# Kernel optimization log

Hardware: AMD Instinct MI355X
Metric: run time of the kernel (lower is better)

The kernel has to match this reference:

```python
import jax, jax.numpy as jnp
import numpy as np

B, T, D = 4096, 200, 64
NEG_INF = -(2.0 ** 32) + 1.0  # matches tf paddings constant


def setup_inputs() -> dict:
    key = jax.random.key(0)
    ks = jax.random.split(key, 12)
    queries = jax.random.normal(ks[0], (B, D), dtype=jnp.float32)
    keys = jax.random.normal(ks[1], (B, T, D), dtype=jnp.float32)
    keys_length = jax.random.randint(ks[2], (B,), 0, 200, dtype=jnp.int32)
    # attention MLP params (glorot-ish scale)
    W1 = jax.random.normal(ks[3], (4 * D, 16), dtype=jnp.float32) * (1.0 / np.sqrt(4 * D))
    b1 = jnp.zeros((16,), dtype=jnp.float32)
    W2 = jax.random.normal(ks[4], (16, 8), dtype=jnp.float32) * (1.0 / np.sqrt(16))
    b2 = jnp.zeros((8,), dtype=jnp.float32)
    W3 = jax.random.normal(ks[5], (8, 1), dtype=jnp.float32) * (1.0 / np.sqrt(8))
    b3 = jnp.zeros((1,), dtype=jnp.float32)
    W4 = jax.random.normal(ks[6], (D, D), dtype=jnp.float32) * (1.0 / np.sqrt(D))
    b4 = jnp.zeros((D,), dtype=jnp.float32)
    return {"queries": queries, "keys": keys, "keys_length": keys_length,
            "W1": W1, "b1": b1, "W2": W2, "b2": b2, "W3": W3, "b3": b3,
            "W4": W4, "b4": b4}


def reference(queries, keys, keys_length, W1, b1, W2, b2, W3, b3, W4, b4):
    Bq, Tq, Dq = keys.shape
    # tile queries across time: [B, T, D]
    q = jnp.broadcast_to(queries[:, None, :], (Bq, Tq, Dq))
    # DIN feature construction: [B, T, 4D]
    din_all = jnp.concatenate([q, keys, q - keys, q * keys], axis=-1)
    # tiny MLP scorer
    x = jax.nn.sigmoid(jnp.einsum('btf,fh->bth', din_all, W1) + b1)
    x = jax.nn.sigmoid(jnp.einsum('bth,hk->btk', x, W2) + b2)
    scores = (jnp.einsum('btk,ko->bto', x, W3) + b3)[..., 0]  # [B, T]
    # mask invalid history positions
    mask = jnp.arange(Tq, dtype=keys_length.dtype)[None, :] < keys_length[:, None]
    scores = jnp.where(mask, scores, NEG_INF)
    scores = scores / (Dq ** 0.5)  # scaling applied after masking, as in tf code
    attn = jax.nn.softmax(scores, axis=-1)  # [B, T]
    out = jnp.einsum('bt,btd->bd', attn, keys)  # weighted sum of keys
    out = out @ W4 + b4  # [B, D]
    return out
```

## Files before the change

kernel.cpp:

```cpp
#include <hip/hip_runtime.h>
#include <math.h>

#define TT 200
#define MTS 72

typedef __attribute__((ext_vector_type(8))) short bf16x8;
typedef __attribute__((ext_vector_type(4))) float f32x4;

__device__ __forceinline__ float sigmoidf_(float x) {
    return 1.0f / (1.0f + __expf(-x));
}
__device__ __forceinline__ short f2bf(float x) {
    unsigned u = __float_as_uint(x);
    u += 0x7fff + ((u >> 16) & 1);
    return (short)(u >> 16);
}
__device__ __forceinline__ float bf2f(short s) {
    return __uint_as_float(((unsigned)(unsigned short)s) << 16);
}
__device__ __forceinline__ void build_hi(float4 v0, float4 v1, bf16x8& hi) {
    float xs[8] = {v0.x, v0.y, v0.z, v0.w, v1.x, v1.y, v1.z, v1.w};
    #pragma unroll
    for (int j = 0; j < 8; j++) hi[j] = f2bf(xs[j]);
}

__global__ __launch_bounds__(256) void din_attn_flash(
    const float* __restrict__ queries,
    const float* __restrict__ keys,
    const int*   __restrict__ keys_length,
    const float* __restrict__ W1,
    const float* __restrict__ b1,
    const float* __restrict__ W2,
    const float* __restrict__ b2,
    const float* __restrict__ W3,
    const float* __restrict__ b3,
    const float* __restrict__ W4,
    const float* __restrict__ b4,
    float* __restrict__ out,
    int Bn)
{
    __shared__ __align__(16) short MtHi[4][16 * MTS];
    __shared__ __align__(16) short MtLo[4][16 * MTS];
    __shared__ __align__(16) float w2s[16 * 8];
    __shared__ __align__(16) float vS[4][64];

    const int tid  = threadIdx.x;
    const int w    = tid >> 6;
    const int lane = tid & 63;
    const int m16  = lane & 15;
    const int quad = lane >> 4;

    if (tid < 128) w2s[tid] = W2[tid];
    __syncthreads();

    const int b = blockIdx.x * 4 + w;
    if (b >= Bn) return;
    const int len = __builtin_amdgcn_readfirstlane(keys_length[b]);
    const float* kb = keys + (size_t)b * (TT * 64);

    float cp0 = 0.f, cp1 = 0.f, cp2 = 0.f, cp3 = 0.f;
    {
        const int d2 = lane >> 2;
        const int hg = lane & 3;
        const float4* W1v = (const float4*)W1;
        #pragma unroll
        for (int dg = 0; dg < 4; dg++) {
            const int d = dg * 16 + d2;
            const float q = queries[b * 64 + d];
            float4 a  = W1v[(0   + d) * 4 + hg];
            float4 bb = W1v[(64  + d) * 4 + hg];
            float4 cc = W1v[(128 + d) * 4 + hg];
            float4 dd = W1v[(192 + d) * 4 + hg];
            float mv0 = bb.x - cc.x + q * dd.x;
            float mv1 = bb.y - cc.y + q * dd.y;
            float mv2 = bb.z - cc.z + q * dd.z;
            float mv3 = bb.w - cc.w + q * dd.w;
            cp0 += q * (a.x + cc.x);
            cp1 += q * (a.y + cc.y);
            cp2 += q * (a.z + cc.z);
            cp3 += q * (a.w + cc.w);
            const int hb = hg * 4;
            short h0 = f2bf(mv0), h1 = f2bf(mv1), h2 = f2bf(mv2), h3 = f2bf(mv3);
            MtHi[w][(hb + 0) * MTS + d] = h0;
            MtHi[w][(hb + 1) * MTS + d] = h1;
            MtHi[w][(hb + 2) * MTS + d] = h2;
            MtHi[w][(hb + 3) * MTS + d] = h3;
            MtLo[w][(hb + 0) * MTS + d] = f2bf(mv0 - bf2f(h0));
            MtLo[w][(hb + 1) * MTS + d] = f2bf(mv1 - bf2f(h1));
            MtLo[w][(hb + 2) * MTS + d] = f2bf(mv2 - bf2f(h2));
            MtLo[w][(hb + 3) * MTS + d] = f2bf(mv3 - bf2f(h3));
        }
        #pragma unroll
        for (int mask = 4; mask <= 32; mask <<= 1) {
            cp0 += __shfl_xor(cp0, mask, 64);
            cp1 += __shfl_xor(cp1, mask, 64);
            cp2 += __shfl_xor(cp2, mask, 64);
            cp3 += __shfl_xor(cp3, mask, 64);
        }
    }
    float cv4[4];
    cv4[0] = __shfl(cp0, quad, 64) + b1[quad * 4 + 0];
    cv4[1] = __shfl(cp1, quad, 64) + b1[quad * 4 + 1];
    cv4[2] = __shfl(cp2, quad, 64) + b1[quad * 4 + 2];
    cv4[3] = __shfl(cp3, quad, 64) + b1[quad * 4 + 3];

    asm volatile("" ::: "memory");
    __builtin_amdgcn_wave_barrier();

    const int bb0 = m16 * MTS + quad * 8;
    const bf16x8 Bh0 = *(const bf16x8*)&MtHi[w][bb0];
    const bf16x8 Bh1 = *(const bf16x8*)&MtHi[w][bb0 + 32];
    const bf16x8 Bl0 = *(const bf16x8*)&MtLo[w][bb0];
    const bf16x8 Bl1 = *(const bf16x8*)&MtLo[w][bb0 + 32];

    const float4* w2s4 = (const float4*)w2s;
    const float4 b2a = *(const float4*)(b2);
    const float4 b2b = *(const float4*)(b2 + 4);
    const float4 w3a = *(const float4*)(W3);
    const float4 w3b = *(const float4*)(W3 + 4);
    const float  b3v = b3[0];

    float mrun = -3.0e38f;
    float ssum = 0.0f;
    float o[16];
    #pragma unroll
    for (int j = 0; j < 16; j++) o[j] = 0.0f;

    const int ntiles = (len == 0) ? 13 : ((len + 15) >> 4);

    const float* kp0 = kb + m16 * 64 + quad * 8;
    float4 c0 = *(const float4*)(kp0);
    float4 c1 = *(const float4*)(kp0 + 4);
    float4 c2 = *(const float4*)(kp0 + 32);
    float4 c3 = *(const float4*)(kp0 + 36);

    for (int tile = 0; tile < ntiles; tile++) {
        float4 n0, n1, n2, n3;
        const bool pf = (tile + 1 < ntiles);
        if (pf) {
            int tr = (tile + 1) * 16 + m16;
            if (tr > TT - 1) tr = TT - 1;
            const float* np = kb + tr * 64 + quad * 8;
            n0 = *(const float4*)(np);
            n1 = *(const float4*)(np + 4);
            n2 = *(const float4*)(np + 32);
            n3 = *(const float4*)(np + 36);
        }
        bf16x8 ah0, ah1;
        build_hi(c0, c1, ah0);
        build_hi(c2, c3, ah1);
        f32x4 acc = {0.f, 0.f, 0.f, 0.f};
        acc = __builtin_amdgcn_mfma_f32_16x16x32_bf16(Bh0, ah0, acc, 0, 0, 0);
        acc = __builtin_amdgcn_mfma_f32_16x16x32_bf16(Bl0, ah0, acc, 0, 0, 0);
        acc = __builtin_amdgcn_mfma_f32_16x16x32_bf16(Bh1, ah1, acc, 0, 0, 0);
        acc = __builtin_amdgcn_mfma_f32_16x16x32_bf16(Bl1, ah1, acc, 0, 0, 0);

        float s2[8] = {b2a.x, b2a.y, b2a.z, b2a.w, b2b.x, b2b.y, b2b.z, b2b.w};
        #pragma unroll
        for (int r = 0; r < 4; r++) {
            const float h1 = sigmoidf_(acc[r] + cv4[r]);
            const float4 wa = w2s4[(quad * 4 + r) * 2];
            const float4 wb = w2s4[(quad * 4 + r) * 2 + 1];
            s2[0] = fmaf(h1, wa.x, s2[0]);
            s2[1] = fmaf(h1, wa.y, s2[1]);
            s2[2] = fmaf(h1, wa.z, s2[2]);
            s2[3] = fmaf(h1, wa.w, s2[3]);
            s2[4] = fmaf(h1, wb.x, s2[4]);
            s2[5] = fmaf(h1, wb.y, s2[5]);
            s2[6] = fmaf(h1, wb.z, s2[6]);
            s2[7] = fmaf(h1, wb.w, s2[7]);
        }
        #pragma unroll
        for (int j = 0; j < 8; j++) {
            s2[j] += __shfl_xor(s2[j], 16, 64);
            s2[j] += __shfl_xor(s2[j], 32, 64);
        }
        float s3 = b3v;
        s3 = fmaf(sigmoidf_(s2[0]), w3a.x, s3);
        s3 = fmaf(sigmoidf_(s2[1]), w3a.y, s3);
        s3 = fmaf(sigmoidf_(s2[2]), w3a.z, s3);
        s3 = fmaf(sigmoidf_(s2[3]), w3a.w, s3);
        s3 = fmaf(sigmoidf_(s2[4]), w3b.x, s3);
        s3 = fmaf(sigmoidf_(s2[5]), w3b.y, s3);
        s3 = fmaf(sigmoidf_(s2[6]), w3b.z, s3);
        s3 = fmaf(sigmoidf_(s2[7]), w3b.w, s3);

        const int tg = tile * 16 + m16;
        float sc = s3 * 0.125f;
        if (tg >= len) sc = -536870912.0f;
        if (tg >= TT)  sc = -INFINITY;

        float mx = sc;
        mx = fmaxf(mx, __shfl_xor(mx, 1, 64));
        mx = fmaxf(mx, __shfl_xor(mx, 2, 64));
        mx = fmaxf(mx, __shfl_xor(mx, 4, 64));
        mx = fmaxf(mx, __shfl_xor(mx, 8, 64));
        const float mnew = fmaxf(mrun, mx);
        const float fr = __expf(mrun - mnew);
        const float p  = __expf(sc - mnew);
        mrun = mnew;
        float ps = p;
        ps += __shfl_xor(ps, 1, 64);
        ps += __shfl_xor(ps, 2, 64);
        ps += __shfl_xor(ps, 4, 64);
        ps += __shfl_xor(ps, 8, 64);
        ssum = fmaf(ssum, fr, ps);
        o[0]  = fmaf(o[0],  fr, p * c0.x);
        o[1]  = fmaf(o[1],  fr, p * c0.y);
        o[2]  = fmaf(o[2],  fr, p * c0.z);
        o[3]  = fmaf(o[3],  fr, p * c0.w);
        o[4]  = fmaf(o[4],  fr, p * c1.x);
        o[5]  = fmaf(o[5],  fr, p * c1.y);
        o[6]  = fmaf(o[6],  fr, p * c1.z);
        o[7]  = fmaf(o[7],  fr, p * c1.w);
        o[8]  = fmaf(o[8],  fr, p * c2.x);
        o[9]  = fmaf(o[9],  fr, p * c2.y);
        o[10] = fmaf(o[10], fr, p * c2.z);
        o[11] = fmaf(o[11], fr, p * c2.w);
        o[12] = fmaf(o[12], fr, p * c3.x);
        o[13] = fmaf(o[13], fr, p * c3.y);
        o[14] = fmaf(o[14], fr, p * c3.z);
        o[15] = fmaf(o[15], fr, p * c3.w);

        if (pf) { c0 = n0; c1 = n1; c2 = n2; c3 = n3; }
    }

    #pragma unroll
    for (int mask = 1; mask <= 8; mask <<= 1) {
        #pragma unroll
        for (int j = 0; j < 16; j++) o[j] += __shfl_xor(o[j], mask, 64);
    }
    const float inv = 1.0f / ssum;
    if (m16 == 0) {
        #pragma unroll
        for (int j = 0; j < 8; j++) vS[w][quad * 8 + j]      = o[j] * inv;
        #pragma unroll
        for (int j = 0; j < 8; j++) vS[w][32 + quad * 8 + j] = o[8 + j] * inv;
    }
    asm volatile("" ::: "memory");
    __builtin_amdgcn_wave_barrier();

    float po = b4[lane];
    const float4* vS4 = (const float4*)&vS[w][0];
    #pragma unroll 4
    for (int d0 = 0; d0 < 16; d0++) {
        const float4 vv = vS4[d0];
        const float* w4p = W4 + d0 * 256 + lane;
        po = fmaf(vv.x, w4p[0],   po);
        po = fmaf(vv.y, w4p[64],  po);
        po = fmaf(vv.z, w4p[128], po);
        po = fmaf(vv.w, w4p[192], po);
    }
    out[(size_t)b * 64 + lane] = po;
}

extern "C" void kernel_launch(void* const* d_in, const int* in_sizes, int n_in,
                              void* d_out, int out_size, void* d_ws, size_t ws_size,
                              hipStream_t stream) {
    const float* queries     = (const float*)d_in[0];
    const float* keys        = (const float*)d_in[1];
    const int*   keys_length = (const int*)  d_in[2];
    const float* W1 = (const float*)d_in[3];
    const float* b1 = (const float*)d_in[4];
    const float* W2 = (const float*)d_in[5];
    const float* b2 = (const float*)d_in[6];
    const float* W3 = (const float*)d_in[7];
    const float* b3 = (const float*)d_in[8];
    const float* W4 = (const float*)d_in[9];
    const float* b4 = (const float*)d_in[10];
    float* out = (float*)d_out;

    const int Bn = in_sizes[2];
    const int blocks = (Bn + 3) >> 2;
    din_attn_flash<<<blocks, 256, 0, stream>>>(
        queries, keys, keys_length, W1, b1, W2, b2, W3, b3, W4, b4, out, Bn);
}
```

Baseline: 304.7 us.

## Replace online softmax with fixed analytic max bound and hoist W2 into registers

The score is a sigmoid-weighted sum, so its magnitude is bounded by |b3| plus the sum of |W3|. The change uses that bound as a fixed softmax offset, removing the per-tile running max, rescale factors, and per-tile shuffle reductions. The sum reduction is deferred until after the loop. W2 rows are loaded into registers instead of shared memory, which removes a block-wide __syncthreads. The fully masked (len==0) case is handled as a uniform distribution over all T. The cost is more live registers.

```diff
diff --git a/kernel.cpp b/kernel.cpp
--- a/kernel.cpp
+++ b/kernel.cpp
@@ -41,7 +41,6 @@
 {
     __shared__ __align__(16) short MtHi[4][16 * MTS];
     __shared__ __align__(16) short MtLo[4][16 * MTS];
-    __shared__ __align__(16) float w2s[16 * 8];
     __shared__ __align__(16) float vS[4][64];
 
     const int tid  = threadIdx.x;
@@ -49,9 +48,6 @@
     const int lane = tid & 63;
     const int m16  = lane & 15;
     const int quad = lane >> 4;
-
-    if (tid < 128) w2s[tid] = W2[tid];
-    __syncthreads();
 
     const int b = blockIdx.x * 4 + w;
     if (b >= Bn) return;
@@ -113,20 +109,29 @@
     const bf16x8 Bl0 = *(const bf16x8*)&MtLo[w][bb0];
     const bf16x8 Bl1 = *(const bf16x8*)&MtLo[w][bb0 + 32];
 
-    const float4* w2s4 = (const float4*)w2s;
+    float4 wa_[4], wb_[4];
+    #pragma unroll
+    for (int r = 0; r < 4; r++) {
+        wa_[r] = *(const float4*)(W2 + (quad * 4 + r) * 8);
+        wb_[r] = *(const float4*)(W2 + (quad * 4 + r) * 8 + 4);
+    }
     const float4 b2a = *(const float4*)(b2);
     const float4 b2b = *(const float4*)(b2 + 4);
     const float4 w3a = *(const float4*)(W3);
     const float4 w3b = *(const float4*)(W3 + 4);
     const float  b3v = b3[0];
 
-    float mrun = -3.0e38f;
+    const float M = 0.125f * (fabsf(b3v)
+                  + fabsf(w3a.x) + fabsf(w3a.y) + fabsf(w3a.z) + fabsf(w3a.w)
+                  + fabsf(w3b.x) + fabsf(w3b.y) + fabsf(w3b.z) + fabsf(w3b.w));
+
+    const int lenEff = (len == 0) ? TT : len;
+    const int ntiles = (lenEff + 15) >> 4;
+
     float ssum = 0.0f;
     float o[16];
     #pragma unroll
     for (int j = 0; j < 16; j++) o[j] = 0.0f;
-
-    const int ntiles = (len == 0) ? 13 : ((len + 15) >> 4);
 
     const float* kp0 = kb + m16 * 64 + quad * 8;
     float4 c0 = *(const float4*)(kp0);
@@ -159,16 +164,14 @@
         #pragma unroll
         for (int r = 0; r < 4; r++) {
             const float h1 = sigmoidf_(acc[r] + cv4[r]);
-            const float4 wa = w2s4[(quad * 4 + r) * 2];
-            const float4 wb = w2s4[(quad * 4 + r) * 2 + 1];
-            s2[0] = fmaf(h1, wa.x, s2[0]);
-            s2[1] = fmaf(h1, wa.y, s2[1]);
-            s2[2] = fmaf(h1, wa.z, s2[2]);
-            s2[3] = fmaf(h1, wa.w, s2[3]);
-            s2[4] = fmaf(h1, wb.x, s2[4]);
-            s2[5] = fmaf(h1, wb.y, s2[5]);
-            s2[6] = fmaf(h1, wb.z, s2[6]);
-            s2[7] = fmaf(h1, wb.w, s2[7]);
+            s2[0] = fmaf(h1, wa_[r].x, s2[0]);
+            s2[1] = fmaf(h1, wa_[r].y, s2[1]);
+            s2[2] = fmaf(h1, wa_[r].z, s2[2]);
+            s2[3] = fmaf(h1, wa_[r].w, s2[3]);
+            s2[4] = fmaf(h1, wb_[r].x, s2[4]);
+            s2[5] = fmaf(h1, wb_[r].y, s2[5]);
+            s2[6] = fmaf(h1, wb_[r].z, s2[6]);
+            s2[7] = fmaf(h1, wb_[r].w, s2[7]);
         }
         #pragma unroll
         for (int j = 0; j < 8; j++) {
@@ -186,47 +189,34 @@
         s3 = fmaf(sigmoidf_(s2[7]), w3b.w, s3);
 
         const int tg = tile * 16 + m16;
-        float sc = s3 * 0.125f;
-        if (tg >= len) sc = -536870912.0f;
-        if (tg >= TT)  sc = -INFINITY;
-
-        float mx = sc;
-        mx = fmaxf(mx, __shfl_xor(mx, 1, 64));
-        mx = fmaxf(mx, __shfl_xor(mx, 2, 64));
-        mx = fmaxf(mx, __shfl_xor(mx, 4, 64));
-        mx = fmaxf(mx, __shfl_xor(mx, 8, 64));
-        const float mnew = fmaxf(mrun, mx);
-        const float fr = __expf(mrun - mnew);
-        const float p  = __expf(sc - mnew);
-        mrun = mnew;
-        float ps = p;
-        ps += __shfl_xor(ps, 1, 64);
-        ps += __shfl_xor(ps, 2, 64);
-        ps += __shfl_xor(ps, 4, 64);
-        ps += __shfl_xor(ps, 8, 64);
-        ssum = fmaf(ssum, fr, ps);
-        o[0]  = fmaf(o[0],  fr, p * c0.x);
-        o[1]  = fmaf(o[1],  fr, p * c0.y);
-        o[2]  = fmaf(o[2],  fr, p * c0.z);
-        o[3]  = fmaf(o[3],  fr, p * c0.w);
-        o[4]  = fmaf(o[4],  fr, p * c1.x);
-        o[5]  = fmaf(o[5],  fr, p * c1.y);
-        o[6]  = fmaf(o[6],  fr, p * c1.z);
-        o[7]  = fmaf(o[7],  fr, p * c1.w);
-        o[8]  = fmaf(o[8],  fr, p * c2.x);
-        o[9]  = fmaf(o[9],  fr, p * c2.y);
-        o[10] = fmaf(o[10], fr, p * c2.z);
-        o[11] = fmaf(o[11], fr, p * c2.w);
-        o[12] = fmaf(o[12], fr, p * c3.x);
-        o[13] = fmaf(o[13], fr, p * c3.y);
-        o[14] = fmaf(o[14], fr, p * c3.z);
-        o[15] = fmaf(o[15], fr, p * c3.w);
+        float sc = (len == 0) ? 0.0f : s3 * 0.125f;
+        if (tg >= lenEff) sc = -1.0e30f;
+        const float p = __expf(sc - M);
+
+        ssum += p;
+        o[0]  = fmaf(p, c0.x, o[0]);
+        o[1]  = fmaf(p, c0.y, o[1]);
+        o[2]  = fmaf(p, c0.z, o[2]);
+        o[3]  = fmaf(p, c0.w, o[3]);
+        o[4]  = fmaf(p, c1.x, o[4]);
+        o[5]  = fmaf(p, c1.y, o[5]);
+        o[6]  = fmaf(p, c1.z, o[6]);
+        o[7]  = fmaf(p, c1.w, o[7]);
+        o[8]  = fmaf(p, c2.x, o[8]);
+        o[9]  = fmaf(p, c2.y, o[9]);
+        o[10] = fmaf(p, c2.z, o[10]);
+        o[11] = fmaf(p, c2.w, o[11]);
+        o[12] = fmaf(p, c3.x, o[12]);
+        o[13] = fmaf(p, c3.y, o[13]);
+        o[14] = fmaf(p, c3.z, o[14]);
+        o[15] = fmaf(p, c3.w, o[15]);
 
         if (pf) { c0 = n0; c1 = n1; c2 = n2; c3 = n3; }
     }
 
     #pragma unroll
     for (int mask = 1; mask <= 8; mask <<= 1) {
+        ssum += __shfl_xor(ssum, mask, 64);
         #pragma unroll
         for (int j = 0; j < 16; j++) o[j] += __shfl_xor(o[j], mask, 64);
     }
```

Result: faster. 294.5 us (-3.4%).
